# Optimization experiments

Measured on AMD Instinct MI355X. Metric: run time of the kernel, lower is better.

The kernel has to match this reference:

```python
import jax, jax.numpy as jnp
import numpy as np


def setup_inputs() -> dict:
    key = jax.random.key(0)
    ks = jax.random.split(key, 4)
    B, T, D, U = 32, 1024, 1024, 1024
    x = jax.random.normal(ks[0], (B, T, D), dtype=jnp.float32)
    W = jax.random.normal(ks[1], (D, 4 * U), dtype=jnp.float32) * (1.0 / np.sqrt(D))
    b = jnp.zeros((4 * U,), dtype=jnp.float32)
    Vr = jax.random.normal(ks[2], (U,), dtype=jnp.float32) * 0.1
    Vf = jax.random.normal(ks[3], (U,), dtype=jnp.float32) * 0.1
    h0 = jnp.zeros((B, U), dtype=jnp.float32)
    c0 = jnp.zeros((B, U), dtype=jnp.float32)
    return {"x": x, "h0": h0, "c0": c0, "W": W, "b": b, "Vr": Vr, "Vf": Vf}


def _sru(x, h0, c0, W, b, Vr, Vf):
    B, T, D = x.shape
    U = Vr.shape[0]
    # Batched matmul across all timesteps, then sequential elementwise scan.
    g = jnp.einsum('btd,dk->btk', x, W) + b            # [B, T, 4U]
    g = jnp.moveaxis(g, 1, 0)                          # [T, B, 4U]
    g1, g2, g3, g4 = jnp.split(g, 4, axis=-1)          # each [T, B, U]

    def step(c_, gs):
        a1, a2, a3, a4 = gs
        f = jax.nn.sigmoid(a1 + Vf * c_)
        c = f * c_ + (1.0 - f) * a2
        r = jax.nn.sigmoid(a3 + Vr * c_)
        h = r * c + (1.0 - r) * a4
        return c, h

    c_last, hs = jax.lax.scan(step, c0, (g1, g2, g3, g4))
    return jnp.moveaxis(hs, 0, 1)                      # [B, T, U]


def reference(x, h0, c0, W, b, Vr, Vf):
    return _sru(x, h0, c0, W, b, Vr, Vf)
```

## Files before the change

kernel.cpp:

```cpp
#include <hip/hip_runtime.h>
#include <cstdint>
#include <cstddef>

typedef short short8 __attribute__((ext_vector_type(8)));
typedef short s16x4 __attribute__((ext_vector_type(4)));
typedef float f32x4 __attribute__((ext_vector_type(4)));

typedef const __attribute__((address_space(1))) void* gas_ptr;
typedef __attribute__((address_space(3))) void* las_ptr;

__device__ __forceinline__ unsigned short f2bf(float f) {
    unsigned int u = __float_as_uint(f);
    u += 0x7fffu + ((u >> 16) & 1u);
    return (unsigned short)(u >> 16);
}
__device__ __forceinline__ float bf2f(unsigned short s) {
    return __uint_as_float(((unsigned int)s) << 16);
}
__device__ __forceinline__ float sigmoid_f(float z) {
    return __builtin_amdgcn_rcpf(1.0f + __expf(-z));
}
__device__ __forceinline__ void async_copy16(const void* gp, void* lp) {
    __builtin_amdgcn_global_load_lds((gas_ptr)gp, (las_ptr)lp, 16, 0, 0);
}

__global__ __launch_bounds__(256) void cvt_x_kernel(const float* __restrict__ in,
                                                    unsigned short* __restrict__ out) {
    size_t i = ((size_t)blockIdx.x * 256 + threadIdx.x) * 8;
    float4 v0 = *(const float4*)(in + i);
    float4 v1 = *(const float4*)(in + i + 4);
    short8 o;
    o[0]=(short)f2bf(v0.x); o[1]=(short)f2bf(v0.y); o[2]=(short)f2bf(v0.z); o[3]=(short)f2bf(v0.w);
    o[4]=(short)f2bf(v1.x); o[5]=(short)f2bf(v1.y); o[6]=(short)f2bf(v1.z); o[7]=(short)f2bf(v1.w);
    *(short8*)(out + i) = o;
}

__global__ __launch_bounds__(256) void cvt_w_kernel(const float* __restrict__ W,
                                                    unsigned short* __restrict__ Wt) {
    __shared__ unsigned short tile[64][65];
    int bk = blockIdx.x >> 6, bn = blockIdx.x & 63;
    int k0 = bk * 64, n0 = bn * 64;
    int t = threadIdx.x;
    int cr = t >> 6;
    int cc = t & 63;
#pragma unroll
    for (int i = 0; i < 16; ++i) {
        int row = i * 4 + cr;
        tile[row][cc] = f2bf(W[(size_t)(k0 + row) * 4096 + n0 + cc]);
    }
    __syncthreads();
#pragma unroll
    for (int i = 0; i < 16; ++i) {
        int nrow = i * 4 + cr;
        Wt[(size_t)(n0 + nrow) * 1024 + k0 + cc] = tile[cc][nrow];
    }
}

__global__ __launch_bounds__(256, 2) void gemm_kernel(const unsigned short* __restrict__ A,
                                                      const unsigned short* __restrict__ Bt,
                                                      const float* __restrict__ bias,
                                                      unsigned short* __restrict__ gT) {
    __shared__ __align__(16) unsigned short As[128 * 64];
    __shared__ __align__(16) unsigned short Bs[128 * 64];

    int bid = blockIdx.x;
    int band = bid >> 8;
    int r = bid & 255;
    int mt = band * 8 + (r >> 5);
    int nt = r & 31;
    int m0 = mt * 128, n0 = nt * 128;

    int tidx = threadIdx.x;
    int lane = tidx & 63, wv = tidx >> 6;
    int wm = wv >> 1, wn = wv & 1;
    int l15 = lane & 15, quad = lane >> 4;

    f32x4 acc[4][4] = {};

    for (int k0 = 0; k0 < 1024; k0 += 64) {
        __syncthreads();
#pragma unroll
        for (int i = 0; i < 4; ++i) {
            int ci = (wv * 4 + i) * 64 + lane;
            int row = ci >> 3, cc = ci & 7;
            int sc = (cc ^ (row & 7)) << 3;
            const unsigned short* ga = A + (size_t)(m0 + row) * 1024 + k0 + sc;
            async_copy16(ga, (char*)As + (wv * 4 + i) * 1024);
            const unsigned short* gb = Bt + (size_t)(n0 + row) * 1024 + k0 + sc;
            async_copy16(gb, (char*)Bs + (wv * 4 + i) * 1024);
        }
        __syncthreads();
#pragma unroll
        for (int kt = 0; kt < 2; ++kt) {
            short8 af[4], bf[4];
#pragma unroll
            for (int mt2 = 0; mt2 < 4; ++mt2) {
                int row = wm * 64 + mt2 * 16 + l15;
                int kc = kt * 4 + quad;
                af[mt2] = *(const short8*)((const char*)As + row * 128 + ((kc ^ (row & 7)) << 4));
            }
#pragma unroll
            for (int nt2 = 0; nt2 < 4; ++nt2) {
                int rown = wn * 64 + nt2 * 16 + l15;
                int kc = kt * 4 + quad;
                bf[nt2] = *(const short8*)((const char*)Bs + rown * 128 + ((kc ^ (rown & 7)) << 4));
            }
#pragma unroll
            for (int mt2 = 0; mt2 < 4; ++mt2)
#pragma unroll
                for (int nt2 = 0; nt2 < 4; ++nt2)
                    acc[mt2][nt2] = __builtin_amdgcn_mfma_f32_16x16x32_bf16(
                        af[mt2], bf[nt2], acc[mt2][nt2], 0, 0, 0);
        }
    }

#pragma unroll
    for (int mt2 = 0; mt2 < 4; ++mt2) {
        int mbase = m0 + wm * 64 + mt2 * 16 + quad * 4;
        int b_ = mbase >> 10, t_ = mbase & 1023;
#pragma unroll
        for (int nt2 = 0; nt2 < 4; ++nt2) {
            int n = n0 + wn * 64 + nt2 * 16 + l15;
            int gate = n >> 10, u = n & 1023;
            float bv = bias[n];
            s16x4 pk;
            pk[0] = (short)f2bf(acc[mt2][nt2][0] + bv);
            pk[1] = (short)f2bf(acc[mt2][nt2][1] + bv);
            pk[2] = (short)f2bf(acc[mt2][nt2][2] + bv);
            pk[3] = (short)f2bf(acc[mt2][nt2][3] + bv);
            size_t off = ((((size_t)(t_ >> 3) * 32 + (size_t)b_) * 4 + (size_t)gate) << 13)
                         + ((size_t)u << 3) + (size_t)(t_ & 7);
            *(s16x4*)(gT + off) = pk;
        }
    }
}

__global__ __launch_bounds__(512, 4) void scan_kernel(const unsigned short* __restrict__ gT,
                                                      const float* __restrict__ c0,
                                                      const float* __restrict__ Vr,
                                                      const float* __restrict__ Vf,
                                                      float* __restrict__ h) {
    __shared__ __align__(16) unsigned short sbuf[2 * 4 * 8 * 512];

    const int NCH = 16;
    int blk = blockIdx.x;
    int b = blk >> 4;
    int u0 = (blk & 15) << 6;
    int tid = threadIdx.x;
    int wv = tid >> 6;
    int lane = tid & 63;

    size_t gbase = (size_t)b * 32768 + ((size_t)(u0 + lane) << 3);

    if (wv >= 1) {
        for (int p = wv - 1; p < 32; p += 7) {
            int gate = p >> 3, tbi = p & 7;
            const unsigned short* src = gT + ((size_t)tbi << 20) + gbase + gate * 8192;
            char* dst = (char*)sbuf + gate * 8192 + tbi * 1024 + lane * 16;
            async_copy16(src, dst);
        }
    }
    __syncthreads();

    float c = 0.0f, vf = 0.0f, vr = 0.0f;
    float* hb = nullptr;
    if (wv == 0) {
        int u = u0 + lane;
        c = c0[(b << 10) + u];
        vf = Vf[u];
        vr = Vr[u];
        hb = h + ((size_t)b << 20) + u;
    }

    for (int k = 0; k < NCH; ++k) {
        if (wv >= 1) {
            if (k + 1 < NCH) {
                int nb = (k + 1) & 1;
                for (int p = wv - 1; p < 32; p += 7) {
                    int gate = p >> 3, tbi = p & 7;
                    const unsigned short* src =
                        gT + ((size_t)((k + 1) * 8 + tbi) << 20) + gbase + gate * 8192;
                    char* dst = (char*)sbuf + nb * 32768 + gate * 8192 + tbi * 1024 + lane * 16;
                    async_copy16(src, dst);
                }
            }
        } else {
            const unsigned short* ls = sbuf + (k & 1) * 16384 + (size_t)lane * 8;
#pragma unroll
            for (int tbi = 0; tbi < 8; ++tbi) {
                short8 a1 = *(const short8*)(ls + tbi * 512);
                short8 a2 = *(const short8*)(ls + 4096 + tbi * 512);
                short8 a3 = *(const short8*)(ls + 8192 + tbi * 512);
                short8 a4 = *(const short8*)(ls + 12288 + tbi * 512);
                int t0 = (k * 8 + tbi) * 8;
#pragma unroll
                for (int i = 0; i < 8; ++i) {
                    float x1 = bf2f((unsigned short)a1[i]);
                    float x2 = bf2f((unsigned short)a2[i]);
                    float x3 = bf2f((unsigned short)a3[i]);
                    float x4 = bf2f((unsigned short)a4[i]);
                    float f  = sigmoid_f(x1 + vf * c);
                    float cp = c;
                    c = fmaf(f, c - x2, x2);
                    float rr = sigmoid_f(x3 + vr * cp);
                    float hv = fmaf(rr, c - x4, x4);
                    hb[(size_t)(t0 + i) << 10] = hv;
                }
            }
        }
        __syncthreads();
    }
}

extern "C" void kernel_launch(void* const* d_in, const int* in_sizes, int n_in,
                              void* d_out, int out_size, void* d_ws, size_t ws_size,
                              hipStream_t stream) {
    const float* x  = (const float*)d_in[0];
    const float* c0 = (const float*)d_in[2];
    const float* W  = (const float*)d_in[3];
    const float* b  = (const float*)d_in[4];
    const float* Vr = (const float*)d_in[5];
    const float* Vf = (const float*)d_in[6];
    float* h = (float*)d_out;

    char* ws = (char*)d_ws;
    unsigned short* xb = (unsigned short*)ws;
    unsigned short* wt = (unsigned short*)(ws + (size_t)67108864);
    unsigned short* gT = (unsigned short*)(ws + (size_t)75497472);

    cvt_x_kernel<<<16384, 256, 0, stream>>>(x, xb);
    cvt_w_kernel<<<1024, 256, 0, stream>>>(W, wt);
    gemm_kernel<<<8192, 256, 0, stream>>>(xb, wt, b, gT);
    scan_kernel<<<512, 512, 0, stream>>>(gT, c0, Vr, Vf, h);
}
```

Baseline: 562.6 us.

## Offload scan output stores to dedicated writer waves via LDS staging

The compute wave now writes h values into a double-buffered LDS tile rather than issuing strided global stores itself. Three separate waves then flush the previous chunk to global memory while the next chunk is being computed. Chunks shrink from 64 to 32 timesteps so that LDS usage stays about the same with the added h buffer. __syncthreads is replaced by a raw s_barrier plus explicit waitcnt. The intent is to take global store latency off the sequential recurrence's critical path, at the cost of twice as many barriers.

```diff
diff --git a/kernel.cpp b/kernel.cpp
--- a/kernel.cpp
+++ b/kernel.cpp
@@ -140,9 +140,10 @@
                                                       const float* __restrict__ Vr,
                                                       const float* __restrict__ Vf,
                                                       float* __restrict__ h) {
-    __shared__ __align__(16) unsigned short sbuf[2 * 4 * 8 * 512];
-
-    const int NCH = 16;
+    __shared__ __align__(16) unsigned short sbuf[2 * 4 * 4 * 512];
+    __shared__ __align__(16) float hbuf[2][32][64];
+
+    const int NCH = 32;
     int blk = blockIdx.x;
     int b = blk >> 4;
     int u0 = (blk & 15) << 6;
@@ -152,47 +153,35 @@
 
     size_t gbase = (size_t)b * 32768 + ((size_t)(u0 + lane) << 3);
 
-    if (wv >= 1) {
-        for (int p = wv - 1; p < 32; p += 7) {
-            int gate = p >> 3, tbi = p & 7;
+    if (wv >= 1 && wv <= 4) {
+        for (int p = wv - 1; p < 16; p += 4) {
+            int gate = p >> 2, tbi = p & 3;
             const unsigned short* src = gT + ((size_t)tbi << 20) + gbase + gate * 8192;
-            char* dst = (char*)sbuf + gate * 8192 + tbi * 1024 + lane * 16;
+            char* dst = (char*)sbuf + gate * 4096 + tbi * 1024 + lane * 16;
             async_copy16(src, dst);
         }
-    }
-    __syncthreads();
+        asm volatile("s_waitcnt vmcnt(0)" ::: "memory");
+    }
+    __builtin_amdgcn_s_barrier();
 
     float c = 0.0f, vf = 0.0f, vr = 0.0f;
-    float* hb = nullptr;
     if (wv == 0) {
         int u = u0 + lane;
         c = c0[(b << 10) + u];
         vf = Vf[u];
         vr = Vr[u];
-        hb = h + ((size_t)b << 20) + u;
-    }
+    }
+    float* hb = h + ((size_t)b << 20) + u0 + lane;
 
     for (int k = 0; k < NCH; ++k) {
-        if (wv >= 1) {
-            if (k + 1 < NCH) {
-                int nb = (k + 1) & 1;
-                for (int p = wv - 1; p < 32; p += 7) {
-                    int gate = p >> 3, tbi = p & 7;
-                    const unsigned short* src =
-                        gT + ((size_t)((k + 1) * 8 + tbi) << 20) + gbase + gate * 8192;
-                    char* dst = (char*)sbuf + nb * 32768 + gate * 8192 + tbi * 1024 + lane * 16;
-                    async_copy16(src, dst);
-                }
-            }
-        } else {
-            const unsigned short* ls = sbuf + (k & 1) * 16384 + (size_t)lane * 8;
-#pragma unroll
-            for (int tbi = 0; tbi < 8; ++tbi) {
+        if (wv == 0) {
+            const unsigned short* ls = sbuf + (k & 1) * 8192 + (size_t)lane * 8;
+#pragma unroll
+            for (int tbi = 0; tbi < 4; ++tbi) {
                 short8 a1 = *(const short8*)(ls + tbi * 512);
-                short8 a2 = *(const short8*)(ls + 4096 + tbi * 512);
-                short8 a3 = *(const short8*)(ls + 8192 + tbi * 512);
-                short8 a4 = *(const short8*)(ls + 12288 + tbi * 512);
-                int t0 = (k * 8 + tbi) * 8;
+                short8 a2 = *(const short8*)(ls + 2048 + tbi * 512);
+                short8 a3 = *(const short8*)(ls + 4096 + tbi * 512);
+                short8 a4 = *(const short8*)(ls + 6144 + tbi * 512);
 #pragma unroll
                 for (int i = 0; i < 8; ++i) {
                     float x1 = bf2f((unsigned short)a1[i]);
@@ -204,11 +193,42 @@
                     c = fmaf(f, c - x2, x2);
                     float rr = sigmoid_f(x3 + vr * cp);
                     float hv = fmaf(rr, c - x4, x4);
-                    hb[(size_t)(t0 + i) << 10] = hv;
+                    hbuf[k & 1][tbi * 8 + i][lane] = hv;
                 }
             }
-        }
-        __syncthreads();
+            asm volatile("s_waitcnt lgkmcnt(0)" ::: "memory");
+        } else if (wv <= 4) {
+            if (k + 1 < NCH) {
+                int nb = (k + 1) & 1;
+                for (int p = wv - 1; p < 16; p += 4) {
+                    int gate = p >> 2, tbi = p & 3;
+                    const unsigned short* src =
+                        gT + ((size_t)((k + 1) * 4 + tbi) << 20) + gbase + gate * 8192;
+                    char* dst = (char*)sbuf + nb * 16384 + gate * 4096 + tbi * 1024 + lane * 16;
+                    async_copy16(src, dst);
+                }
+            }
+            asm volatile("s_waitcnt vmcnt(0)" ::: "memory");
+        } else {
+            if (k > 0) {
+                int cb = (k - 1) & 1;
+                int tg0 = (k - 1) * 32;
+                for (int t = wv - 5; t < 32; t += 3) {
+                    float v = hbuf[cb][t][lane];
+                    hb[(size_t)(tg0 + t) << 10] = v;
+                }
+            }
+        }
+        __builtin_amdgcn_s_barrier();
+    }
+
+    if (wv >= 5) {
+        int cb = (NCH - 1) & 1;
+        int tg0 = (NCH - 1) * 32;
+        for (int t = wv - 5; t < 32; t += 3) {
+            float v = hbuf[cb][t][lane];
+            hb[(size_t)(tg0 + t) << 10] = v;
+        }
     }
 }
 
```

After: 565.2 us. About the same (+0.5%).
